# Optimization experiments

Measured on AMD Instinct MI355X. Metric: run time of the kernel, lower is better.

## Reference

```python
import jax, jax.numpy as jnp
import numpy as np

BATCH = 2048
INPUT_DIM = 512
N = 8 ** 4  # reservoir_n ** reservoir_d = 4096
T = 16
NEG_SLOPE = 0.1
SPARSITY = 0.1  # fraction of nonzero entries in the pre-trained reservoir W


def setup_inputs() -> dict:
    key = jax.random.key(0)
    kx, kw, km = jax.random.split(key, 3)
    x = jax.random.normal(kx, (BATCH, INPUT_DIM), dtype=jnp.float32)
    # Sparse pre-trained reservoir weights; scale keeps spectral norm ~O(1)
    # so the T-step recurrence neither explodes nor vanishes.
    mask = (jax.random.uniform(km, (N, N)) < SPARSITY).astype(jnp.float32)
    W = jax.random.normal(kw, (N, N), dtype=jnp.float32) * mask / jnp.sqrt(SPARSITY * N)
    return {"x": x, "W": W}


def reference(x, W):
    # Pad input [B, input_dim] -> initial state S [B, N]
    S0 = jnp.pad(x, ((0, 0), (0, N - x.shape[1])))

    def step(S, _):
        S = jax.nn.leaky_relu(S @ W, negative_slope=NEG_SLOPE)
        return S, None

    S_final, _ = jax.lax.scan(step, S0, None, length=T)
    return S_final
```

## Files before the change

kernel.cpp:

```cpp
#include <hip/hip_runtime.h>


#define BATCH 2048
#define NDIM  4096
#define INDIM 512
#define BM 128
#define BN 128
#define BK 32

typedef _Float16 f16x8 __attribute__((ext_vector_type(8)));
typedef float    f32x4 __attribute__((ext_vector_type(4)));

__device__ __forceinline__ void async16(const void* gsrc, void* ldst) {
  const __attribute__((address_space(1))) unsigned int* g =
      (const __attribute__((address_space(1))) unsigned int*)gsrc;
  __attribute__((address_space(3))) unsigned int* l =
      (__attribute__((address_space(3))) unsigned int*)ldst;
  __builtin_amdgcn_global_load_lds(g, l, 16, 0, 0);
}

#define WAITV0() do { asm volatile("s_waitcnt vmcnt(0)" ::: "memory"); \
                      __builtin_amdgcn_sched_barrier(0); } while (0)
#define SBAR()   __builtin_amdgcn_s_barrier()

__global__ void prep_x(const float* __restrict__ x,
                       _Float16* __restrict__ Sh, _Float16* __restrict__ Sl) {
  size_t i = (size_t)blockIdx.x * 256 + threadIdx.x;
  int b = (int)(i >> 12);
  int n = (int)(i & (NDIM - 1));
  float v = (n < INDIM) ? x[(size_t)b * INDIM + n] : 0.0f;
  _Float16 h = (_Float16)v;
  Sh[i] = h;
  Sl[i] = (_Float16)(v - (float)h);
}

__global__ void prep_w(const float* __restrict__ W,
                       _Float16* __restrict__ Wth, _Float16* __restrict__ Wtl) {
  __shared__ float tile[32][33];
  int k0 = blockIdx.y * 32, n0 = blockIdx.x * 32;
  int tx = threadIdx.x, ty = threadIdx.y;
  for (int r = 0; r < 4; r++) {
    int k = k0 + ty + r * 8;
    tile[ty + r * 8][tx] = W[(size_t)k * NDIM + n0 + tx];
  }
  __syncthreads();
  for (int r = 0; r < 4; r++) {
    int n = n0 + ty + r * 8;
    float v = tile[tx][ty + r * 8] * 256.0f;
    _Float16 h = (_Float16)v;
    Wth[(size_t)n * NDIM + k0 + tx] = h;
    Wtl[(size_t)n * NDIM + k0 + tx] = (_Float16)(v - (float)h);
  }
}

#define READF(b)                                       \
  do {                                                 \
    _Pragma("unroll") for (int i = 0; i < 4; i++) {    \
      af[i] = *(const f16x8*)&sAh[b][oA[i]];           \
      lf[i] = *(const f16x8*)&sAl[b][oA[i]];           \
    }                                                  \
    _Pragma("unroll") for (int j = 0; j < 2; j++) {    \
      bf[j] = *(const f16x8*)&sBh[b][oB[j]];           \
      mf[j] = *(const f16x8*)&sBl[b][oB[j]];           \
    }                                                  \
  } while (0)

#define MFMAS()                                                                     \
  do {                                                                              \
    _Pragma("unroll") for (int j = 0; j < 2; j++)                                   \
    _Pragma("unroll") for (int i = 0; i < 4; i++)                                   \
      acc[i][j] = __builtin_amdgcn_mfma_f32_16x16x32_f16(af[i], bf[j], acc[i][j], 0, 0, 0); \
    _Pragma("unroll") for (int j = 0; j < 2; j++)                                   \
    _Pragma("unroll") for (int i = 0; i < 4; i++)                                   \
      acc[i][j] = __builtin_amdgcn_mfma_f32_16x16x32_f16(lf[i], bf[j], acc[i][j], 0, 0, 0); \
    _Pragma("unroll") for (int j = 0; j < 2; j++)                                   \
    _Pragma("unroll") for (int i = 0; i < 4; i++)                                   \
      acc[i][j] = __builtin_amdgcn_mfma_f32_16x16x32_f16(af[i], mf[j], acc[i][j], 0, 0, 0); \
  } while (0)

template <int MODE>
__global__ __launch_bounds__(512, 4) void step_kernel(
    const _Float16* __restrict__ Ah, const _Float16* __restrict__ Al,
    const _Float16* __restrict__ Bh, const _Float16* __restrict__ Bl,
    _Float16* __restrict__ Dh, _Float16* __restrict__ Dl,
    float* __restrict__ Dout, int k_len) {
  __shared__ _Float16 sAh[2][BM * BK];
  __shared__ _Float16 sAl[2][BM * BK];
  __shared__ _Float16 sBh[2][BN * BK];
  __shared__ _Float16 sBl[2][BN * BK];

  const int tid = threadIdx.x;
  const int lane = tid & 63;
  const int w = tid >> 6;
  const int wm = w >> 2, wn = w & 3;

  int id = blockIdx.x;
  int xcd = id & 7, local = id >> 3;
  int lr = local & 7, lc = local >> 3;
  const int bm = ((xcd & 1) * 8 + lr) * BM;
  const int bn = ((xcd >> 1) * 8 + lc) * BN;

  const int sr = lane >> 2, cl = lane & 3;
  const int fm = lane & 15, fq = lane >> 4;

  int oA[4], oB[2];
#pragma unroll
  for (int i = 0; i < 4; i++) {
    int rA = wm * 64 + i * 16 + fm;
    oA[i] = rA * BK + (fq ^ ((rA >> 1) & 3)) * 8;
  }
#pragma unroll
  for (int j = 0; j < 2; j++) {
    int rB = wn * 32 + j * 16 + fm;
    oB[j] = rB * BK + (fq ^ ((rB >> 1) & 3)) * 8;
  }

  int r0 = w * 16 + sr;
  int cg0 = cl ^ ((r0 >> 1) & 3);
  const size_t gA0 = (size_t)(bm + r0) * NDIM + cg0 * 8;
  const size_t gB0 = (size_t)(bn + r0) * NDIM + cg0 * 8;
  const int lo0 = r0 * BK + cl * 8;

  auto stage = [&](int kt, int b) {
    async16(Ah + gA0 + kt, &sAh[b][lo0]);
    async16(Al + gA0 + kt, &sAl[b][lo0]);
    async16(Bh + gB0 + kt, &sBh[b][lo0]);
    async16(Bl + gB0 + kt, &sBl[b][lo0]);
  };

  f32x4 acc[4][2];
#pragma unroll
  for (int i = 0; i < 4; i++)
#pragma unroll
    for (int j = 0; j < 2; j++) acc[i][j] = (f32x4){0.f, 0.f, 0.f, 0.f};

  f16x8 af[4], lf[4], bf[2], mf[2];

  const int nk = k_len / BK;

  stage(0 * BK, 0);
  for (int it = 0; it < nk; ++it) {
    const int p = it & 1;
    WAITV0();
    SBAR();
    if (it + 1 < nk) stage((it + 1) * BK, p ^ 1);
    READF(p);
    MFMAS();
  }

  const float inv = 1.0f / 256.0f;
#pragma unroll
  for (int i = 0; i < 4; i++) {
#pragma unroll
    for (int j = 0; j < 2; j++) {
#pragma unroll
      for (int e = 0; e < 4; e++) {
        int r = bm + wm * 64 + i * 16 + fq * 4 + e;
        int c = bn + wn * 32 + j * 16 + fm;
        float g = acc[i][j][e] * inv;
        float s = (g > 0.0f) ? g : 0.1f * g;
        if (MODE == 0) {
          _Float16 h = (_Float16)s;
          Dh[(size_t)r * NDIM + c] = h;
          Dl[(size_t)r * NDIM + c] = (_Float16)(s - (float)h);
        } else {
          Dout[(size_t)r * NDIM + c] = s;
        }
      }
    }
  }
}

extern "C" void kernel_launch(void* const* d_in, const int* in_sizes, int n_in,
                              void* d_out, int out_size, void* d_ws, size_t ws_size,
                              hipStream_t stream) {
  const float* x = (const float*)d_in[0];
  const float* W = (const float*)d_in[1];
  float* out = (float*)d_out;
  char* ws = (char*)d_ws;

  const size_t WT_BYTES = (size_t)NDIM * NDIM * 2;
  const size_t S_BYTES = (size_t)BATCH * NDIM * 2;
  _Float16* Wth = (_Float16*)ws;
  _Float16* Wtl = (_Float16*)(ws + WT_BYTES);
  _Float16* SAh = (_Float16*)(ws + 2 * WT_BYTES);
  _Float16* SAl = (_Float16*)(ws + 2 * WT_BYTES + S_BYTES);
  _Float16* SBh = (_Float16*)(ws + 2 * WT_BYTES + 2 * S_BYTES);
  _Float16* SBl = (_Float16*)(ws + 2 * WT_BYTES + 3 * S_BYTES);

  prep_x<<<(BATCH * NDIM) / 256, 256, 0, stream>>>(x, SAh, SAl);
  prep_w<<<dim3(NDIM / 32, NDIM / 32), dim3(32, 8), 0, stream>>>(W, Wth, Wtl);

  dim3 grid((NDIM / BN) * (BATCH / BM));
  for (int t = 1; t <= 16; t++) {
    const _Float16* ah = (t & 1) ? SAh : SBh;
    const _Float16* al = (t & 1) ? SAl : SBl;
    _Float16* dh = (t & 1) ? SBh : SAh;
    _Float16* dl = (t & 1) ? SBl : SAl;
    int klen = (t == 1) ? INDIM : NDIM;
    if (t < 16)
      step_kernel<0><<<grid, 512, 0, stream>>>(ah, al, Wth, Wtl, dh, dl, nullptr, klen);
    else
      step_kernel<1><<<grid, 512, 0, stream>>>(ah, al, Wth, Wtl, nullptr, nullptr, out, klen);
  }
}
```

Before: 2.692 ms.

## Enlarge M tile to 256 and triple-buffer LDS with two-stage prefetch

Doubles the block tile along the batch dimension to 256 rows, so each wave computes 8x2 MFMA tiles and every W tile loaded from memory is reused across twice as many rows. It also switches from double to triple buffering with a two-iteration-ahead prefetch and a partial vmcnt wait, so global loads overlap more compute. The block-to-tile mapping is changed to match the new grid. The cost is much higher register and LDS use, with launch bounds lowered to 2 blocks per CU, so occupancy falls.

New measurement: 3.231 ms. 1.2x slower.

```diff
diff --git a/kernel.cpp b/kernel.cpp
--- a/kernel.cpp
+++ b/kernel.cpp
@@ -4,7 +4,7 @@
 #define BATCH 2048
 #define NDIM  4096
 #define INDIM 512
-#define BM 128
+#define BM 256
 #define BN 128
 #define BK 32
 
@@ -19,6 +19,8 @@
   __builtin_amdgcn_global_load_lds(g, l, 16, 0, 0);
 }
 
+#define WAITV6() do { asm volatile("s_waitcnt vmcnt(6)" ::: "memory"); \
+                      __builtin_amdgcn_sched_barrier(0); } while (0)
 #define WAITV0() do { asm volatile("s_waitcnt vmcnt(0)" ::: "memory"); \
                       __builtin_amdgcn_sched_barrier(0); } while (0)
 #define SBAR()   __builtin_amdgcn_s_barrier()
@@ -53,41 +55,45 @@
   }
 }
 
-#define READF(b)                                       \
+#define READF(p)                                       \
   do {                                                 \
-    _Pragma("unroll") for (int i = 0; i < 4; i++) {    \
-      af[i] = *(const f16x8*)&sAh[b][oA[i]];           \
-      lf[i] = *(const f16x8*)&sAl[b][oA[i]];           \
+    const _Float16* bAh = &sAh[p][0];                  \
+    const _Float16* bAl = &sAl[p][0];                  \
+    const _Float16* bBh = &sBh[p][0];                  \
+    const _Float16* bBl = &sBl[p][0];                  \
+    _Pragma("unroll") for (int i = 0; i < 8; i++) {    \
+      af[i] = *(const f16x8*)&bAh[oA[i]];              \
+      lf[i] = *(const f16x8*)&bAl[oA[i]];              \
     }                                                  \
     _Pragma("unroll") for (int j = 0; j < 2; j++) {    \
-      bf[j] = *(const f16x8*)&sBh[b][oB[j]];           \
-      mf[j] = *(const f16x8*)&sBl[b][oB[j]];           \
+      bf[j] = *(const f16x8*)&bBh[oB[j]];              \
+      mf[j] = *(const f16x8*)&bBl[oB[j]];              \
     }                                                  \
   } while (0)
 
 #define MFMAS()                                                                     \
   do {                                                                              \
     _Pragma("unroll") for (int j = 0; j < 2; j++)                                   \
-    _Pragma("unroll") for (int i = 0; i < 4; i++)                                   \
+    _Pragma("unroll") for (int i = 0; i < 8; i++)                                   \
       acc[i][j] = __builtin_amdgcn_mfma_f32_16x16x32_f16(af[i], bf[j], acc[i][j], 0, 0, 0); \
     _Pragma("unroll") for (int j = 0; j < 2; j++)                                   \
-    _Pragma("unroll") for (int i = 0; i < 4; i++)                                   \
+    _Pragma("unroll") for (int i = 0; i < 8; i++)                                   \
       acc[i][j] = __builtin_amdgcn_mfma_f32_16x16x32_f16(lf[i], bf[j], acc[i][j], 0, 0, 0); \
     _Pragma("unroll") for (int j = 0; j < 2; j++)                                   \
-    _Pragma("unroll") for (int i = 0; i < 4; i++)                                   \
+    _Pragma("unroll") for (int i = 0; i < 8; i++)                                   \
       acc[i][j] = __builtin_amdgcn_mfma_f32_16x16x32_f16(af[i], mf[j], acc[i][j], 0, 0, 0); \
   } while (0)
 
 template <int MODE>
-__global__ __launch_bounds__(512, 4) void step_kernel(
+__global__ __launch_bounds__(512, 2) void step_kernel(
     const _Float16* __restrict__ Ah, const _Float16* __restrict__ Al,
     const _Float16* __restrict__ Bh, const _Float16* __restrict__ Bl,
     _Float16* __restrict__ Dh, _Float16* __restrict__ Dl,
     float* __restrict__ Dout, int k_len) {
-  __shared__ _Float16 sAh[2][BM * BK];
-  __shared__ _Float16 sAl[2][BM * BK];
-  __shared__ _Float16 sBh[2][BN * BK];
-  __shared__ _Float16 sBl[2][BN * BK];
+  __shared__ _Float16 sAh[3][BM * BK];
+  __shared__ _Float16 sAl[3][BM * BK];
+  __shared__ _Float16 sBh[3][BN * BK];
+  __shared__ _Float16 sBl[3][BN * BK];
 
   const int tid = threadIdx.x;
   const int lane = tid & 63;
@@ -96,17 +102,16 @@
 
   int id = blockIdx.x;
   int xcd = id & 7, local = id >> 3;
-  int lr = local & 7, lc = local >> 3;
-  const int bm = ((xcd & 1) * 8 + lr) * BM;
-  const int bn = ((xcd >> 1) * 8 + lc) * BN;
+  const int bm = (local & 7) * BM;
+  const int bn = (xcd * 4 + (local >> 3)) * BN;
 
   const int sr = lane >> 2, cl = lane & 3;
   const int fm = lane & 15, fq = lane >> 4;
 
-  int oA[4], oB[2];
-#pragma unroll
-  for (int i = 0; i < 4; i++) {
-    int rA = wm * 64 + i * 16 + fm;
+  int oA[8], oB[2];
+#pragma unroll
+  for (int i = 0; i < 8; i++) {
+    int rA = wm * 128 + i * 16 + fm;
     oA[i] = rA * BK + (fq ^ ((rA >> 1) & 3)) * 8;
   }
 #pragma unroll
@@ -115,47 +120,60 @@
     oB[j] = rB * BK + (fq ^ ((rB >> 1) & 3)) * 8;
   }
 
-  int r0 = w * 16 + sr;
+  int r0 = w * 32 + sr, r1 = r0 + 16;
+  int rb = w * 16 + sr;
   int cg0 = cl ^ ((r0 >> 1) & 3);
+  int cg1 = cl ^ ((r1 >> 1) & 3);
+  int cgB = cl ^ ((rb >> 1) & 3);
   const size_t gA0 = (size_t)(bm + r0) * NDIM + cg0 * 8;
-  const size_t gB0 = (size_t)(bn + r0) * NDIM + cg0 * 8;
+  const size_t gA1 = (size_t)(bm + r1) * NDIM + cg1 * 8;
+  const size_t gB0 = (size_t)(bn + rb) * NDIM + cgB * 8;
   const int lo0 = r0 * BK + cl * 8;
+  const int lo1 = r1 * BK + cl * 8;
+  const int loB = rb * BK + cl * 8;
 
   auto stage = [&](int kt, int b) {
     async16(Ah + gA0 + kt, &sAh[b][lo0]);
+    async16(Ah + gA1 + kt, &sAh[b][lo1]);
     async16(Al + gA0 + kt, &sAl[b][lo0]);
-    async16(Bh + gB0 + kt, &sBh[b][lo0]);
-    async16(Bl + gB0 + kt, &sBl[b][lo0]);
+    async16(Al + gA1 + kt, &sAl[b][lo1]);
+    async16(Bh + gB0 + kt, &sBh[b][loB]);
+    async16(Bl + gB0 + kt, &sBl[b][loB]);
   };
 
-  f32x4 acc[4][2];
-#pragma unroll
-  for (int i = 0; i < 4; i++)
+  f32x4 acc[8][2];
+#pragma unroll
+  for (int i = 0; i < 8; i++)
 #pragma unroll
     for (int j = 0; j < 2; j++) acc[i][j] = (f32x4){0.f, 0.f, 0.f, 0.f};
 
-  f16x8 af[4], lf[4], bf[2], mf[2];
+  f16x8 af[8], lf[8], bf[2], mf[2];
 
   const int nk = k_len / BK;
 
   stage(0 * BK, 0);
+  stage(1 * BK, 1);
+  int p = 0;
   for (int it = 0; it < nk; ++it) {
-    const int p = it & 1;
-    WAITV0();
+    if (it + 1 < nk) { WAITV6(); } else { WAITV0(); }
     SBAR();
-    if (it + 1 < nk) stage((it + 1) * BK, p ^ 1);
+    if (it + 2 < nk) {
+      int q = (p == 0) ? 2 : p - 1;
+      stage((it + 2) * BK, q);
+    }
     READF(p);
     MFMAS();
+    p = (p == 2) ? 0 : p + 1;
   }
 
   const float inv = 1.0f / 256.0f;
 #pragma unroll
-  for (int i = 0; i < 4; i++) {
+  for (int i = 0; i < 8; i++) {
 #pragma unroll
     for (int j = 0; j < 2; j++) {
 #pragma unroll
       for (int e = 0; e < 4; e++) {
-        int r = bm + wm * 64 + i * 16 + fq * 4 + e;
+        int r = bm + wm * 128 + i * 16 + fq * 4 + e;
         int c = bn + wn * 32 + j * 16 + fm;
         float g = acc[i][j][e] * inv;
         float s = (g > 0.0f) ? g : 0.1f * g;
```

## Widen N tile to 256, triple-buffer LDS, interleave staging with MFMA quarters

Applied to the files above, without the earlier changes.

Doubles the per-block N tile so each warp computes a 64x64 sub-tile, which raises the ratio of MFMA work to LDS loads. The shared-memory ring goes from two to three stages, with partial vmcnt waits so loads run two k-steps ahead. Each k-step is split into four quarter phases that interleave LDS fragment reads, async global staging and setprio-raised MFMA groups. This trades occupancy (launch bounds drop to 2 blocks/CU, more LDS and accumulator registers) and adds extra barriers per k-step in exchange for better latency hiding.

Result: slower. 3.029 ms (+12.5%).

```diff
diff --git a/kernel.cpp b/kernel.cpp
--- a/kernel.cpp
+++ b/kernel.cpp
@@ -5,7 +5,7 @@
 #define NDIM  4096
 #define INDIM 512
 #define BM 128
-#define BN 128
+#define BN 256
 #define BK 32
 
 typedef _Float16 f16x8 __attribute__((ext_vector_type(8)));
@@ -19,7 +19,11 @@
   __builtin_amdgcn_global_load_lds(g, l, 16, 0, 0);
 }
 
+#define WAITV6() do { asm volatile("s_waitcnt vmcnt(6)" ::: "memory"); \
+                      __builtin_amdgcn_sched_barrier(0); } while (0)
 #define WAITV0() do { asm volatile("s_waitcnt vmcnt(0)" ::: "memory"); \
+                      __builtin_amdgcn_sched_barrier(0); } while (0)
+#define LGKM0()  do { asm volatile("s_waitcnt lgkmcnt(0)" ::: "memory"); \
                       __builtin_amdgcn_sched_barrier(0); } while (0)
 #define SBAR()   __builtin_amdgcn_s_barrier()
 
@@ -53,41 +57,50 @@
   }
 }
 
-#define READF(b)                                       \
-  do {                                                 \
-    _Pragma("unroll") for (int i = 0; i < 4; i++) {    \
-      af[i] = *(const f16x8*)&sAh[b][oA[i]];           \
-      lf[i] = *(const f16x8*)&sAl[b][oA[i]];           \
-    }                                                  \
-    _Pragma("unroll") for (int j = 0; j < 2; j++) {    \
-      bf[j] = *(const f16x8*)&sBh[b][oB[j]];           \
-      mf[j] = *(const f16x8*)&sBl[b][oB[j]];           \
-    }                                                  \
+#define READQ(b, h, c)                                  \
+  do {                                                  \
+    const _Float16* pAh = &sAh[b][0];                   \
+    const _Float16* pAl = &sAl[b][0];                   \
+    const _Float16* pBh = &sBh[b][0];                   \
+    const _Float16* pBl = &sBl[b][0];                   \
+    af[0] = *(const f16x8*)&pAh[oA[(h)*2 + 0]];         \
+    af[1] = *(const f16x8*)&pAh[oA[(h)*2 + 1]];         \
+    lf[0] = *(const f16x8*)&pAl[oA[(h)*2 + 0]];         \
+    lf[1] = *(const f16x8*)&pAl[oA[(h)*2 + 1]];         \
+    bf[0] = *(const f16x8*)&pBh[oB[(c)*2 + 0]];         \
+    bf[1] = *(const f16x8*)&pBh[oB[(c)*2 + 1]];         \
+    mf[0] = *(const f16x8*)&pBl[oB[(c)*2 + 0]];         \
+    mf[1] = *(const f16x8*)&pBl[oB[(c)*2 + 1]];         \
   } while (0)
 
-#define MFMAS()                                                                     \
-  do {                                                                              \
-    _Pragma("unroll") for (int j = 0; j < 2; j++)                                   \
-    _Pragma("unroll") for (int i = 0; i < 4; i++)                                   \
-      acc[i][j] = __builtin_amdgcn_mfma_f32_16x16x32_f16(af[i], bf[j], acc[i][j], 0, 0, 0); \
-    _Pragma("unroll") for (int j = 0; j < 2; j++)                                   \
-    _Pragma("unroll") for (int i = 0; i < 4; i++)                                   \
-      acc[i][j] = __builtin_amdgcn_mfma_f32_16x16x32_f16(lf[i], bf[j], acc[i][j], 0, 0, 0); \
-    _Pragma("unroll") for (int j = 0; j < 2; j++)                                   \
-    _Pragma("unroll") for (int i = 0; i < 4; i++)                                   \
-      acc[i][j] = __builtin_amdgcn_mfma_f32_16x16x32_f16(af[i], mf[j], acc[i][j], 0, 0, 0); \
+#define MFMAQ(h, c)                                                                  \
+  do {                                                                               \
+    __builtin_amdgcn_s_setprio(1);                                                   \
+    _Pragma("unroll") for (int jj = 0; jj < 2; jj++)                                 \
+    _Pragma("unroll") for (int ii = 0; ii < 2; ii++)                                 \
+      acc[(h)*2+ii][(c)*2+jj] = __builtin_amdgcn_mfma_f32_16x16x32_f16(              \
+          af[ii], bf[jj], acc[(h)*2+ii][(c)*2+jj], 0, 0, 0);                         \
+    _Pragma("unroll") for (int jj = 0; jj < 2; jj++)                                 \
+    _Pragma("unroll") for (int ii = 0; ii < 2; ii++)                                 \
+      acc[(h)*2+ii][(c)*2+jj] = __builtin_amdgcn_mfma_f32_16x16x32_f16(              \
+          lf[ii], bf[jj], acc[(h)*2+ii][(c)*2+jj], 0, 0, 0);                         \
+    _Pragma("unroll") for (int jj = 0; jj < 2; jj++)                                 \
+    _Pragma("unroll") for (int ii = 0; ii < 2; ii++)                                 \
+      acc[(h)*2+ii][(c)*2+jj] = __builtin_amdgcn_mfma_f32_16x16x32_f16(              \
+          af[ii], mf[jj], acc[(h)*2+ii][(c)*2+jj], 0, 0, 0);                         \
+    __builtin_amdgcn_s_setprio(0);                                                   \
   } while (0)
 
 template <int MODE>
-__global__ __launch_bounds__(512, 4) void step_kernel(
+__global__ __launch_bounds__(512, 2) void step_kernel(
     const _Float16* __restrict__ Ah, const _Float16* __restrict__ Al,
     const _Float16* __restrict__ Bh, const _Float16* __restrict__ Bl,
     _Float16* __restrict__ Dh, _Float16* __restrict__ Dl,
     float* __restrict__ Dout, int k_len) {
-  __shared__ _Float16 sAh[2][BM * BK];
-  __shared__ _Float16 sAl[2][BM * BK];
-  __shared__ _Float16 sBh[2][BN * BK];
-  __shared__ _Float16 sBl[2][BN * BK];
+  __shared__ _Float16 sAh[3][BM * BK];
+  __shared__ _Float16 sAl[3][BM * BK];
+  __shared__ _Float16 sBh[3][BN * BK];
+  __shared__ _Float16 sBl[3][BN * BK];
 
   const int tid = threadIdx.x;
   const int lane = tid & 63;
@@ -96,67 +109,104 @@
 
   int id = blockIdx.x;
   int xcd = id & 7, local = id >> 3;
-  int lr = local & 7, lc = local >> 3;
-  const int bm = ((xcd & 1) * 8 + lr) * BM;
-  const int bn = ((xcd >> 1) * 8 + lc) * BN;
-
-  const int sr = lane >> 2, cl = lane & 3;
+  const int bm = (local & 15) * BM;
+  const int bn = (xcd * 2 + (local >> 4)) * BN;
+
   const int fm = lane & 15, fq = lane >> 4;
 
-  int oA[4], oB[2];
+  int oA[4], oB[4];
 #pragma unroll
   for (int i = 0; i < 4; i++) {
     int rA = wm * 64 + i * 16 + fm;
     oA[i] = rA * BK + (fq ^ ((rA >> 1) & 3)) * 8;
   }
 #pragma unroll
-  for (int j = 0; j < 2; j++) {
-    int rB = wn * 32 + j * 16 + fm;
+  for (int j = 0; j < 4; j++) {
+    int rB = wn * 64 + j * 16 + fm;
     oB[j] = rB * BK + (fq ^ ((rB >> 1) & 3)) * 8;
   }
 
-  int r0 = w * 16 + sr;
-  int cg0 = cl ^ ((r0 >> 1) & 3);
+  const int r0 = tid >> 2, cl = tid & 3;
+  const int cg0 = cl ^ ((r0 >> 1) & 3);
+  const int r1 = r0 + 128;
+  const int cg1 = cl ^ ((r1 >> 1) & 3);
   const size_t gA0 = (size_t)(bm + r0) * NDIM + cg0 * 8;
   const size_t gB0 = (size_t)(bn + r0) * NDIM + cg0 * 8;
+  const size_t gB1 = (size_t)(bn + r1) * NDIM + cg1 * 8;
   const int lo0 = r0 * BK + cl * 8;
-
-  auto stage = [&](int kt, int b) {
-    async16(Ah + gA0 + kt, &sAh[b][lo0]);
-    async16(Al + gA0 + kt, &sAl[b][lo0]);
-    async16(Bh + gB0 + kt, &sBh[b][lo0]);
-    async16(Bl + gB0 + kt, &sBl[b][lo0]);
-  };
-
-  f32x4 acc[4][2];
+  const int lo1 = r1 * BK + cl * 8;
+
+  auto stageBh = [&](int koff, int b) {
+    async16(Bh + gB0 + koff, &sBh[b][lo0]);
+    async16(Bh + gB1 + koff, &sBh[b][lo1]);
+  };
+  auto stageBl = [&](int koff, int b) {
+    async16(Bl + gB0 + koff, &sBl[b][lo0]);
+    async16(Bl + gB1 + koff, &sBl[b][lo1]);
+  };
+  auto stageA = [&](int koff, int b) {
+    async16(Ah + gA0 + koff, &sAh[b][lo0]);
+    async16(Al + gA0 + koff, &sAl[b][lo0]);
+  };
+  auto stageFull = [&](int koff, int b) {
+    stageBh(koff, b); stageBl(koff, b); stageA(koff, b);
+  };
+
+  f32x4 acc[4][4];
 #pragma unroll
   for (int i = 0; i < 4; i++)
 #pragma unroll
-    for (int j = 0; j < 2; j++) acc[i][j] = (f32x4){0.f, 0.f, 0.f, 0.f};
-
-  f16x8 af[4], lf[4], bf[2], mf[2];
+    for (int j = 0; j < 4; j++) acc[i][j] = (f32x4){0.f, 0.f, 0.f, 0.f};
+
+  f16x8 af[2], lf[2], bf[2], mf[2];
 
   const int nk = k_len / BK;
 
-  stage(0 * BK, 0);
-  for (int it = 0; it < nk; ++it) {
-    const int p = it & 1;
-    WAITV0();
-    SBAR();
-    if (it + 1 < nk) stage((it + 1) * BK, p ^ 1);
-    READF(p);
-    MFMAS();
+  stageFull(0, 0);
+  stageFull(BK, 1);
+
+  int bufc = 0;
+  for (int kt = 0; kt < nk; ++kt) {
+    const int bufn = (bufc == 0) ? 2 : bufc - 1;
+    const bool st = (kt + 2 < nk);
+    const int ko = (kt + 2) * BK;
+
+    if (kt + 1 < nk) { WAITV6(); } else { WAITV0(); }
+    SBAR();
+    READQ(bufc, 0, 0);
+    if (st) stageBh(ko, bufn);
+    LGKM0();
+    MFMAQ(0, 0);
+
+    SBAR();
+    READQ(bufc, 0, 1);
+    if (st) stageBl(ko, bufn);
+    LGKM0();
+    MFMAQ(0, 1);
+
+    SBAR();
+    READQ(bufc, 1, 0);
+    if (st) stageA(ko, bufn);
+    LGKM0();
+    MFMAQ(1, 0);
+
+    SBAR();
+    READQ(bufc, 1, 1);
+    LGKM0();
+    MFMAQ(1, 1);
+
+    bufc = (bufc == 2) ? 0 : bufc + 1;
   }
 
   const float inv = 1.0f / 256.0f;
 #pragma unroll
   for (int i = 0; i < 4; i++) {
 #pragma unroll
-    for (int j = 0; j < 2; j++) {
+    for (int j = 0; j < 4; j++) {
 #pragma unroll
       for (int e = 0; e < 4; e++) {
         int r = bm + wm * 64 + i * 16 + fq * 4 + e;
-        int c = bn + wn * 32 + j * 16 + fm;
+        int c = bn + wn * 64 + j * 16 + fm;
         float g = acc[i][j][e] * inv;
         float s = (g > 0.0f) ? g : 0.1f * g;
         if (MODE == 0) {
```
